# Kernel tuning notes

Hardware: AMD Instinct MI355X
Metric: run time of the kernel (lower is better)

Reference implementation:

```python
import jax, jax.numpy as jnp
import numpy as np

EPS = 1e-5

def rmsnorm(x, w):
    var = jnp.mean(x * x, axis=-1, keepdims=True)
    return x * jax.lax.rsqrt(var + EPS) * w

def apply_rope(x, cos, sin):
    # x: [B, S, H, D], cos/sin: [S, D//2]; llama-style complex rotation over pairs
    B, S, H, D = x.shape
    xr = x.reshape(B, S, H, D // 2, 2)
    x0, x1 = xr[..., 0], xr[..., 1]
    c = cos[None, :, None, :]
    s = sin[None, :, None, :]
    o0 = x0 * c - x1 * s
    o1 = x0 * s + x1 * c
    return jnp.stack([o0, o1], axis=-1).reshape(B, S, H, D)

def setup_inputs() -> dict:
    key = jax.random.key(0)
    ks = jax.random.split(key, 8)
    B, S, dim = 2, 2048, 2048
    H, nope, rope = 16, 128, 64
    q_lr, kv_lr = 1536, 512
    hd = nope + rope
    x = jax.random.normal(ks[0], (B, S, dim), jnp.float32)
    wd_q = jax.random.normal(ks[1], (dim, q_lr), jnp.float32) * (dim ** -0.5)
    wu_q = jax.random.normal(ks[2], (q_lr, H * hd), jnp.float32) * (q_lr ** -0.5)
    q_norm_w = jnp.ones((q_lr,), jnp.float32)
    wd_kv = jax.random.normal(ks[3], (dim, kv_lr + rope), jnp.float32) * (dim ** -0.5)
    wu_kv = jax.random.normal(ks[4], (kv_lr, H * 2 * nope), jnp.float32) * (kv_lr ** -0.5)
    kv_norm_w = jnp.ones((kv_lr,), jnp.float32)
    wo = jax.random.normal(ks[5], (H * nope, dim), jnp.float32) * ((H * nope) ** -0.5)
    pos = jnp.arange(S, dtype=jnp.float32)
    inv_freq = 1.0 / (10000.0 ** (jnp.arange(0, rope, 2, dtype=jnp.float32) / rope))
    ang = pos[:, None] * inv_freq[None, :]  # [S, rope//2]
    return {"x": x, "wd_q": wd_q, "wu_q": wu_q, "q_norm_w": q_norm_w,
            "wd_kv": wd_kv, "wu_kv": wu_kv, "kv_norm_w": kv_norm_w, "wo": wo,
            "cos": jnp.cos(ang), "sin": jnp.sin(ang), "start_pos": 0}

def reference(x, wd_q, wu_q, q_norm_w, wd_kv, wu_kv, kv_norm_w, wo, cos, sin, start_pos):
    B, S, dim = x.shape
    H, nope, rope = 16, 128, 64
    kv_lr = 512
    hd = nope + rope
    # low-rank Q projection + RMSNorm
    cq = x @ wd_q
    xq = rmsnorm(cq, q_norm_w) @ wu_q
    xq = xq.reshape(B, S, H, hd)
    xq_nope, xq_rope = xq[..., :nope], xq[..., nope:]
    # low-rank KV projection
    kvd = x @ wd_kv
    ckv, xk_rope = kvd[..., :kv_lr], kvd[..., kv_lr:]
    xk_rope = xk_rope.reshape(B, S, 1, rope)
    kvu = (rmsnorm(ckv, kv_norm_w) @ wu_kv).reshape(B, S, H, 2 * nope)
    xk_nope, xv = kvu[..., :nope], kvu[..., nope:]
    # partial RoPE
    xq_rope = apply_rope(xq_rope, cos, sin)
    xk_rope = apply_rope(xk_rope, cos, sin)
    xk_rope = jnp.broadcast_to(xk_rope, (B, S, H, rope))
    q = jnp.concatenate([xq_nope, xq_rope], axis=-1)  # [B,S,H,192]
    k = jnp.concatenate([xk_nope, xk_rope], axis=-1)
    # causal SDPA
    scale = 1.0 / jnp.sqrt(jnp.float32(hd))
    scores = jnp.einsum('bqhd,bkhd->bhqk', q, k) * scale
    mask = jnp.tril(jnp.ones((S, S), bool))
    scores = jnp.where(mask[None, None], scores, jnp.finfo(scores.dtype).min)
    attn = jax.nn.softmax(scores, axis=-1)
    out = jnp.einsum('bhqk,bkhd->bqhd', attn, xv).reshape(B, S, H * nope)
    return out @ wo
```

## Files before the change

kernel.cpp:

```cpp
#include <hip/hip_runtime.h>
#include <hip/hip_bf16.h>

#define S_LEN 2048
#define NHEAD 16
#define NOPE 128
#define ROPE 64
#define HD 192

typedef unsigned short ushort_t;
typedef __attribute__((ext_vector_type(8))) short short8;
typedef __attribute__((ext_vector_type(4))) float f32x4;

#define AS1 __attribute__((address_space(1)))
#define AS3 __attribute__((address_space(3)))

__device__ __forceinline__ unsigned short f2bf(float f) {
  unsigned int u = __float_as_uint(f);
  return (unsigned short)((u + 0x7FFFu + ((u >> 16) & 1u)) >> 16);
}

__global__ __launch_bounds__(256) void prep_k(const float* __restrict__ x, ushort_t* __restrict__ xb,
                                              const float* __restrict__ wd_q, ushort_t* __restrict__ wdqt,
                                              const float* __restrict__ wd_kv, ushort_t* __restrict__ wdkvt,
                                              const float* __restrict__ wu_q, ushort_t* __restrict__ wuqt,
                                              const float* __restrict__ wu_kv, ushort_t* __restrict__ wukvt,
                                              const float* __restrict__ wo, ushort_t* __restrict__ wot) {
  int id = blockIdx.x;
  if (id < 4096) {
    const int i = id * 256 + threadIdx.x;
    const float4 v0 = *(const float4*)&x[(size_t)i * 8];
    const float4 v1 = *(const float4*)&x[(size_t)i * 8 + 4];
    union { uint4 u; ushort_t s[8]; } pk;
    pk.s[0] = f2bf(v0.x); pk.s[1] = f2bf(v0.y); pk.s[2] = f2bf(v0.z); pk.s[3] = f2bf(v0.w);
    pk.s[4] = f2bf(v1.x); pk.s[5] = f2bf(v1.y); pk.s[6] = f2bf(v1.z); pk.s[7] = f2bf(v1.w);
    *(uint4*)&xb[(size_t)i * 8] = pk.u;
    return;
  }
  id -= 4096;
  const float* B; ushort_t* Bt; int K, N, gx;
  if (id < 3072)               { B = wd_q;  Bt = wdqt;  K = 2048; N = 1536; gx = 48;  }
  else if ((id -= 3072) < 1280){ B = wd_kv; Bt = wdkvt; K = 2048; N = 576;  gx = 20;  }
  else if ((id -= 1280) < 4608){ B = wu_q;  Bt = wuqt;  K = 1536; N = 3072; gx = 96;  }
  else if ((id -= 4608) < 2048){ B = wu_kv; Bt = wukvt; K = 512;  N = 4096; gx = 128; }
  else { id -= 2048;             B = wo;    Bt = wot;   K = 2048; N = 2048; gx = 64;  }
  __shared__ float tile[32][33];
  const int tx = threadIdx.x & 31, ty = threadIdx.x >> 5;
  const int n0 = (id % gx) * 32, k0 = (id / gx) * 32;
  if (n0 >= N) {
#pragma unroll
    for (int r = 0; r < 4; ++r)
      Bt[(size_t)(n0 + ty + 8 * r) * K + k0 + tx] = 0;
    return;
  }
#pragma unroll
  for (int r = 0; r < 4; ++r)
    tile[ty + 8 * r][tx] = B[(size_t)(k0 + ty + 8 * r) * N + n0 + tx];
  __syncthreads();
#pragma unroll
  for (int r = 0; r < 4; ++r)
    Bt[(size_t)(n0 + ty + 8 * r) * K + k0 + tx] = f2bf(tile[tx][ty + 8 * r]);
}

template<int EPI>
__global__ __launch_bounds__(512, 4) void mfma_gemm(const ushort_t* __restrict__ A,
                                                 const ushort_t* __restrict__ Bt,
                                                 float* __restrict__ C,
                                                 int M, int N, int K, int ldc,
                                                 ushort_t* __restrict__ kb16o,
                                                 ushort_t* __restrict__ vto,
                                                 float* __restrict__ C2,
                                                 const float* __restrict__ cosb,
                                                 const float* __restrict__ sinb) {
  __shared__ ushort_t As[128 * 32];
  __shared__ ushort_t Bs[128 * 32];
  const int tid = threadIdx.x;
  const int lane = tid & 63;
  const int wave = tid >> 6;
  const int wm = wave & 3, wn = wave >> 2;

  unsigned bxu = blockIdx.x, byu = blockIdx.y;
  {
    const unsigned gx = gridDim.x;
    const unsigned nwg = gx * gridDim.y;
    if ((nwg & 7u) == 0u) {
      unsigned flat = byu * gx + bxu;
      const unsigned cpx = nwg >> 3;
      flat = (flat & 7u) * cpx + (flat >> 3);
      bxu = flat % gx; byu = flat / gx;
    }
  }
  const int m0 = byu * 128, n0 = bxu * 128;
  const int l15 = lane & 15, quad = lane >> 4;

  f32x4 acc[2][4] = {};

  const int ma0 = tid >> 2, kc0 = tid & 3;

  typedef AS3 ushort_t lds_us;
  lds_us* AsL = (lds_us*)As;
  lds_us* BsL = (lds_us*)Bs;
  const int wbase = wave * 512;

  for (int k0 = 0; k0 < K; k0 += 32) {
    __builtin_amdgcn_global_load_lds(
        (const AS1 void*)&A[(size_t)(m0 + ma0) * K + k0 + kc0 * 8],
        (AS3 void*)(AsL + wbase), 16, 0, 0);
    __builtin_amdgcn_global_load_lds(
        (const AS1 void*)&Bt[(size_t)(n0 + ma0) * K + k0 + kc0 * 8],
        (AS3 void*)(BsL + wbase), 16, 0, 0);
    __syncthreads();

    short8 af[2], bf[4];
#pragma unroll
    for (int i = 0; i < 2; ++i)
      af[i] = *(const short8*)&As[(wm * 32 + i * 16 + l15) * 32 + quad * 8];
#pragma unroll
    for (int j = 0; j < 4; ++j)
      bf[j] = *(const short8*)&Bs[(wn * 64 + j * 16 + l15) * 32 + quad * 8];
#pragma unroll
    for (int i = 0; i < 2; ++i)
#pragma unroll
      for (int j = 0; j < 4; ++j)
        acc[i][j] = __builtin_amdgcn_mfma_f32_16x16x32_bf16(af[i], bf[j], acc[i][j], 0, 0, 0);
    __syncthreads();
  }

  if constexpr (EPI == 0) {
#pragma unroll
    for (int i = 0; i < 2; ++i)
#pragma unroll
      for (int r = 0; r < 4; ++r) {
        const size_t rg = (size_t)(m0 + wm * 32 + i * 16 + quad * 4 + r);
#pragma unroll
        for (int j = 0; j < 4; ++j)
          C[rg * ldc + n0 + wn * 64 + j * 16 + l15] = acc[i][j][r];
      }
  } else if constexpr (EPI == 1) {
    const int h = n0 >> 8;
    const bool is_v = (n0 >> 7) & 1;
    if (!is_v) {
#pragma unroll
      for (int i = 0; i < 2; ++i)
#pragma unroll
        for (int r = 0; r < 4; ++r) {
          const size_t rg = (size_t)(m0 + wm * 32 + i * 16 + quad * 4 + r);
#pragma unroll
          for (int j = 0; j < 4; ++j)
            kb16o[rg * 2048 + h * 128 + wn * 64 + j * 16 + l15] = f2bf(acc[i][j][r]);
        }
    } else {
      __shared__ __align__(16) ushort_t trb[64 * 136];
      const int bb = m0 >> 11;
      const int m0loc = m0 & 2047;
      ushort_t* vbase = vto + ((size_t)(bb * NHEAD + h) * 128) * 2048;
#pragma unroll
      for (int vh = 0; vh < 2; ++vh) {
        if (wn == vh) {
#pragma unroll
          for (int i = 0; i < 2; ++i)
#pragma unroll
            for (int r = 0; r < 4; ++r) {
              const int tloc = wm * 32 + i * 16 + quad * 4 + r;
#pragma unroll
              for (int j = 0; j < 4; ++j)
                trb[(j * 16 + l15) * 136 + tloc] = f2bf(acc[i][j][r]);
            }
        }
        __syncthreads();
#pragma unroll
        for (int it = 0; it < 2; ++it) {
          const int u = tid + (it << 9);
          const int vdl = u >> 4, tc = u & 15;
          *(uint4*)&vbase[(size_t)(vh * 64 + vdl) * 2048 + m0loc + tc * 8] =
              *(const uint4*)&trb[vdl * 136 + tc * 8];
        }
        __syncthreads();
      }
    }
  } else if constexpr (EPI == 2) {
    float* Cd;
    int ldd, nc;
    if (n0 < 1536) { Cd = C;  ldd = 1536; nc = n0; }
    else           { Cd = C2; ldd = 640;  nc = n0 - 1536; }
#pragma unroll
    for (int i = 0; i < 2; ++i)
#pragma unroll
      for (int r = 0; r < 4; ++r) {
        const size_t rg = (size_t)(m0 + wm * 32 + i * 16 + quad * 4 + r);
#pragma unroll
        for (int j = 0; j < 4; ++j)
          Cd[rg * ldd + nc + wn * 64 + j * 16 + l15] = acc[i][j][r];
      }
  } else {
    const float qscale = 0.07216878364870323f;
#pragma unroll
    for (int i = 0; i < 2; ++i)
#pragma unroll
      for (int r = 0; r < 4; ++r) {
        const int rg = m0 + wm * 32 + i * 16 + quad * 4 + r;
        const int sp = rg & (S_LEN - 1);
#pragma unroll
        for (int j = 0; j < 4; ++j) {
          const int col = n0 + wn * 64 + j * 16 + l15;
          float val = acc[i][j][r] * qscale;
          const float pr = __shfl_xor(val, 1);
          const int dd = col % HD;
          float o = val;
          if (dd >= NOPE) {
            const int d = (dd - NOPE) >> 1;
            const float cc = cosb[sp * 32 + d];
            const float sn = sinb[sp * 32 + d];
            o = (lane & 1) ? (pr * sn + val * cc) : (val * cc - pr * sn);
          }
          kb16o[(size_t)rg * 3072 + col] = f2bf(o);
        }
      }
  }
}

__global__ __launch_bounds__(256) void rmsnorm2_k(const float* __restrict__ cq,
                                                  ushort_t* __restrict__ cqn,
                                                  const float* __restrict__ qw,
                                                  const float* __restrict__ kvd,
                                                  ushort_t* __restrict__ ckvn,
                                                  const float* __restrict__ kvw,
                                                  ushort_t* __restrict__ krope16,
                                                  const float* __restrict__ cosb,
                                                  const float* __restrict__ sinb) {
  const bool is_q = blockIdx.x < 4096;
  const int row = blockIdx.x & 4095;
  const int tid = threadIdx.x;
  const float* ip = is_q ? cq + (size_t)row * 1536 : kvd + (size_t)row * 640;
  ushort_t* op = is_q ? cqn + (size_t)row * 1536 : ckvn + (size_t)row * 512;
  const float* w = is_q ? qw : kvw;
  const int L = is_q ? 1536 : 512;
  const int nper = L >> 8;
  float r[6];
  float ss = 0.f;
  for (int j = 0; j < nper; ++j) {
    r[j] = ip[tid + (j << 8)];
    ss += r[j] * r[j];
  }
  for (int off = 32; off; off >>= 1) ss += __shfl_down(ss, off);
  __shared__ float wsum[4];
  __shared__ float scale_s;
  if ((tid & 63) == 0) wsum[tid >> 6] = ss;
  __syncthreads();
  if (tid == 0) {
    float t = wsum[0] + wsum[1] + wsum[2] + wsum[3];
    scale_s = rsqrtf(t / (float)L + 1e-5f);
  }
  __syncthreads();
  const float sc = scale_s;
  for (int j = 0; j < nper; ++j)
    op[tid + (j << 8)] = f2bf(r[j] * sc * w[tid + (j << 8)]);
  if (!is_q && tid < 32) {
    const int d = tid;
    const int s = row & (S_LEN - 1);
    const float c = cosb[s * 32 + d];
    const float sn = sinb[s * 32 + d];
    const float* kb = kvd + (size_t)row * 640 + 512;
    const float y0 = kb[2 * d], y1 = kb[2 * d + 1];
    union { unsigned int u; ushort_t s2[2]; } pk;
    pk.s2[0] = f2bf(y0 * c - y1 * sn);
    pk.s2[1] = f2bf(y0 * sn + y1 * c);
    *(unsigned int*)&krope16[(size_t)row * 64 + 2 * d] = pk.u;
  }
}

#define QT 128
#define KC 64
__global__ __launch_bounds__(512, 4) void attn_k(const ushort_t* __restrict__ q16,
                                                 const ushort_t* __restrict__ kb16,
                                                 const ushort_t* __restrict__ vT,
                                                 const ushort_t* __restrict__ krope16,
                                                 ushort_t* __restrict__ outp) {
  const int bx = blockIdx.x;
  const int g = bx & 31;
  const int s = bx >> 5;
  const int tile = (s < 8) ? s : 23 - s;
  const int b = g >> 4, h = g & 15;
  const int q0 = tile * QT;
  const int tid = threadIdx.x;
  const int lane = tid & 63;
  const int wq = tid >> 6;
  const int l15 = lane & 15, quad = lane >> 4;

  __shared__ __align__(16) ushort_t Kn[64 * 128];
  __shared__ __align__(16) ushort_t Kr[64 * 64];
  __shared__ __align__(16) ushort_t Vt[2][128 * 64];
  __shared__ __align__(16) ushort_t Pb[8][16 * 72];

  const int qbase = q0 + wq * 16;
  const size_t growq = (size_t)b * S_LEN + qbase;
  const ushort_t* vTh = vT + ((size_t)(b * NHEAD + h) * 128) * 2048;
  const size_t bbase = (size_t)b * S_LEN;

  typedef AS3 ushort_t lds_us;
  lds_us* KnL = (lds_us*)Kn;
  lds_us* KrL = (lds_us*)Kr;
  lds_us* VtL = (lds_us*)Vt;
  const int wbase = wq * 512;

  auto issueK = [&](int c) {
    const size_t growk = bbase + (size_t)c * KC;
#pragma unroll
    for (int it = 0; it < 2; ++it) {
      const int u = tid + (it << 9);
      const int key = u >> 4, sl = u & 15;
      const int ss = sl ^ (key & 7);
      __builtin_amdgcn_global_load_lds(
          (const AS1 void*)&kb16[(growk + key) * 2048 + h * 128 + ss * 8],
          (AS3 void*)(KnL + wbase + it * 4096), 16, 0, 0);
    }
    {
      const int u = tid;
      const int key = u >> 3, sl = u & 7;
      const int ss = sl ^ (key & 7);
      __builtin_amdgcn_global_load_lds(
          (const AS1 void*)&krope16[(growk + key) * 64 + ss * 8],
          (AS3 void*)(KrL + wbase), 16, 0, 0);
    }
  };
  auto issueV = [&](int c, int buf) {
    const int j0 = c * KC;
#pragma unroll
    for (int it = 0; it < 2; ++it) {
      const int u = tid + (it << 9);
      const int vd = u >> 3, sl = u & 7;
      const int ss = sl ^ (vd & 7);
      __builtin_amdgcn_global_load_lds(
          (const AS1 void*)&vTh[(size_t)vd * 2048 + j0 + ss * 8],
          (AS3 void*)(VtL + buf * 8192 + wbase + it * 4096), 16, 0, 0);
    }
  };

  issueK(0);
  issueV(0, 0);
  __builtin_amdgcn_sched_barrier(0);

  short8 qf[6];
#pragma unroll
  for (int ks = 0; ks < 6; ++ks)
    qf[ks] = *(const short8*)&q16[(growq + l15) * 3072 + h * HD + ks * 32 + quad * 8];

  f32x4 oacc[8] = {};
  float mrow[4], lrow[4];
  int q_r[4];
#pragma unroll
  for (int r = 0; r < 4; ++r) {
    mrow[r] = -1e30f; lrow[r] = 0.f;
    q_r[r] = qbase + quad * 4 + r;
  }

  const int nchunk = (q0 + QT) / KC;

  asm volatile("s_waitcnt vmcnt(2)" ::: "memory");
  __builtin_amdgcn_s_barrier();
  __builtin_amdgcn_sched_barrier(0);

  for (int c = 0; c < nchunk; ++c) {
    const int j0 = c * KC;
    const bool more = (c + 1 < nchunk);
    const int buf = c & 1;
    const bool skipw = (j0 > qbase + 15);

    f32x4 sacc[4] = {};
    if (!skipw) {
      __builtin_amdgcn_s_setprio(1);
#pragma unroll
      for (int ks = 0; ks < 6; ++ks) {
        short8 kf[4];
        if (ks < 4) {
#pragma unroll
          for (int kt = 0; kt < 4; ++kt)
            kf[kt] = *(const short8*)&Kn[(kt * 16 + l15) * 128 + (((ks * 4 + quad) ^ (l15 & 7)) << 3)];
        } else {
#pragma unroll
          for (int kt = 0; kt < 4; ++kt)
            kf[kt] = *(const short8*)&Kr[(kt * 16 + l15) * 64 + ((((ks - 4) * 4 + quad) ^ (l15 & 7)) << 3)];
        }
#pragma unroll
        for (int kt = 0; kt < 4; ++kt)
          sacc[kt] = __builtin_amdgcn_mfma_f32_16x16x32_bf16(qf[ks], kf[kt], sacc[kt], 0, 0, 0);
      }
      __builtin_amdgcn_s_setprio(0);
    }

    __builtin_amdgcn_s_barrier();
    if (more) issueK(c + 1);
    __builtin_amdgcn_sched_barrier(0);

    if (!skipw) {
      if (j0 + KC - 1 > qbase) {
#pragma unroll
        for (int kt = 0; kt < 4; ++kt) {
          const int key = j0 + kt * 16 + l15;
#pragma unroll
          for (int r = 0; r < 4; ++r)
            sacc[kt][r] = (key <= q_r[r]) ? sacc[kt][r] : -1e30f;
        }
      }
      float pmax[4];
#pragma unroll
      for (int r = 0; r < 4; ++r) {
        float mx = fmaxf(fmaxf(sacc[0][r], sacc[1][r]),
                         fmaxf(sacc[2][r], sacc[3][r]));
        mx = fmaxf(mx, __shfl_xor(mx, 1));
        mx = fmaxf(mx, __shfl_xor(mx, 2));
        mx = fmaxf(mx, __shfl_xor(mx, 4));
        mx = fmaxf(mx, __shfl_xor(mx, 8));
        pmax[r] = mx;
      }
      bool need = false;
#pragma unroll
      for (int r = 0; r < 4; ++r)
        need = need || (pmax[r] > mrow[r] + 8.0f);
      const bool upd = __any(need);
      float alpha[4];
      if (upd) {
#pragma unroll
        for (int r = 0; r < 4; ++r) {
          const float mn = fmaxf(mrow[r], pmax[r]);
          alpha[r] = __expf(mrow[r] - mn);
          mrow[r] = mn;
        }
      }
#pragma unroll
      for (int kt = 0; kt < 4; ++kt)
#pragma unroll
        for (int r = 0; r < 4; ++r)
          sacc[kt][r] = __expf(sacc[kt][r] - mrow[r]);
#pragma unroll
      for (int r = 0; r < 4; ++r) {
        float rs = sacc[0][r] + sacc[1][r] + sacc[2][r] + sacc[3][r];
        rs += __shfl_xor(rs, 1);
        rs += __shfl_xor(rs, 2);
        rs += __shfl_xor(rs, 4);
        rs += __shfl_xor(rs, 8);
        lrow[r] = upd ? lrow[r] * alpha[r] + rs : lrow[r] + rs;
      }
#pragma unroll
      for (int kt = 0; kt < 4; ++kt)
#pragma unroll
        for (int r = 0; r < 4; ++r)
          Pb[wq][(quad * 4 + r) * 72 + kt * 16 + l15] = f2bf(sacc[kt][r]);
      if (upd) {
#pragma unroll
        for (int nt = 0; nt < 8; ++nt)
#pragma unroll
          for (int r = 0; r < 4; ++r)
            oacc[nt][r] *= alpha[r];
      }
    }

    if (more) asm volatile("s_waitcnt vmcnt(3)" ::: "memory");
    else      asm volatile("s_waitcnt vmcnt(0)" ::: "memory");
    __builtin_amdgcn_s_barrier();
    __builtin_amdgcn_sched_barrier(0);

    if (!skipw) {
      __builtin_amdgcn_s_setprio(1);
#pragma unroll
      for (int st = 0; st < 2; ++st) {
        const short8 pf = *(const short8*)&Pb[wq][l15 * 72 + st * 32 + quad * 8];
#pragma unroll
        for (int nt = 0; nt < 8; ++nt) {
          const short8 vf = *(const short8*)&Vt[buf][(nt * 16 + l15) * 64 + (((st * 4 + quad) ^ (l15 & 7)) << 3)];
          oacc[nt] = __builtin_amdgcn_mfma_f32_16x16x32_bf16(pf, vf, oacc[nt], 0, 0, 0);
        }
      }
      __builtin_amdgcn_s_setprio(0);
    }

    if (more) {
      issueV(c + 1, buf ^ 1);
      __builtin_amdgcn_sched_barrier(0);
      asm volatile("s_waitcnt vmcnt(2)" ::: "memory");
      __builtin_amdgcn_s_barrier();
      __builtin_amdgcn_sched_barrier(0);
    }
  }

#pragma unroll
  for (int r = 0; r < 4; ++r) {
    const float inv = 1.0f / lrow[r];
    const size_t orow = growq + quad * 4 + r;
#pragma unroll
    for (int nt = 0; nt < 8; ++nt)
      outp[orow * 2048 + h * 128 + nt * 16 + l15] = f2bf(oacc[nt][r] * inv);
  }
}

extern "C" void kernel_launch(void* const* d_in, const int* in_sizes, int n_in,
                              void* d_out, int out_size, void* d_ws, size_t ws_size,
                              hipStream_t stream) {
  const float* x        = (const float*)d_in[0];
  const float* wd_q     = (const float*)d_in[1];
  const float* wu_q     = (const float*)d_in[2];
  const float* q_norm_w = (const float*)d_in[3];
  const float* wd_kv    = (const float*)d_in[4];
  const float* wu_kv    = (const float*)d_in[5];
  const float* kv_norm_w= (const float*)d_in[6];
  const float* wo       = (const float*)d_in[7];
  const float* cosb     = (const float*)d_in[8];
  const float* sinb     = (const float*)d_in[9];
  float* out = (float*)d_out;

  char* ws = (char*)d_ws;
  float*    cq    = (float*)(ws + 0);
  ushort_t* q16   = (ushort_t*)(ws + 0);
  ushort_t* kb16  = (ushort_t*)(ws + 50331648);
  ushort_t* vT    = (ushort_t*)(ws + 67108864);
  ushort_t* xb    = (ushort_t*)(ws + 83886080);
  ushort_t* cqn   = (ushort_t*)(ws + 117440512);
  float*    kvd   = (float*)(ws + 130023424);
  ushort_t* ckvn  = (ushort_t*)(ws + 140509184);
  ushort_t* aoutb = (ushort_t*)(ws + 130023424);
  ushort_t* krope16 = (ushort_t*)(ws + 146800640);
  ushort_t* wdqt  = (ushort_t*)(ws + 147849216);
  ushort_t* wdkvt = (ushort_t*)(ws + 154140672);
  ushort_t* wuqt  = (ushort_t*)(ws + 156762112);
  ushort_t* wukvt = (ushort_t*)(ws + 166199296);
  ushort_t* wot   = (ushort_t*)(ws + 170393600);

  const int M = 2 * S_LEN;
  dim3 blk(256);
  dim3 blk512(512);

  prep_k<<<19200, blk, 0, stream>>>(x, xb, wd_q, wdqt, wd_kv, wdkvt,
                                    wu_q, wuqt, wu_kv, wukvt, wo, wot);

  mfma_gemm<2><<<dim3(2176 / 128, M / 128), blk512, 0, stream>>>(
      xb, wdqt, cq, M, 2176, 2048, 1536, nullptr, nullptr, kvd, nullptr, nullptr);
  rmsnorm2_k<<<2 * M, 256, 0, stream>>>(cq, cqn, q_norm_w, kvd, ckvn, kv_norm_w,
                                        krope16, cosb, sinb);
  mfma_gemm<3><<<dim3(3072 / 128, M / 128), blk512, 0, stream>>>(
      cqn, wuqt, nullptr, M, 3072, 1536, 0, q16, nullptr, nullptr, cosb, sinb);
  mfma_gemm<1><<<dim3(4096 / 128, M / 128), blk512, 0, stream>>>(
      ckvn, wukvt, nullptr, M, 4096, 512, 0, kb16, vT, nullptr, nullptr, nullptr);
  attn_k<<<2 * NHEAD * (S_LEN / QT), 512, 0, stream>>>(q16, kb16, vT, krope16, aoutb);
  mfma_gemm<0><<<dim3(2048 / 128, M / 128), blk512, 0, stream>>>(
      aoutb, wot, out, M, 2048, 2048, 2048, nullptr, nullptr, nullptr, nullptr, nullptr);
}
```

Baseline: 462.6 us.

## Double-buffer GEMM LDS loads with XOR swizzle and MFMA priority

Converts the bf16 MFMA GEMM main loop to a two-stage LDS double buffer, so the next K-slice's global-to-LDS loads are issued before computing on the current slice, with explicit vmcnt waits and barriers. It also XOR-swizzles the column chunk on both the load and fragment-read sides to reduce LDS bank conflicts, and raises wave priority around the MFMA block. LDS use doubles, which may lower occupancy under launch_bounds(512,4), and the hand-written waitcnt and barrier ordering has to be exactly right to stay correct.

```diff
diff --git a/kernel.cpp b/kernel.cpp
--- a/kernel.cpp
+++ b/kernel.cpp
@@ -71,8 +71,8 @@
                                                  float* __restrict__ C2,
                                                  const float* __restrict__ cosb,
                                                  const float* __restrict__ sinb) {
-  __shared__ ushort_t As[128 * 32];
-  __shared__ ushort_t Bs[128 * 32];
+  __shared__ ushort_t As[2][128 * 32];
+  __shared__ ushort_t Bs[2][128 * 32];
   const int tid = threadIdx.x;
   const int lane = tid & 63;
   const int wave = tid >> 6;
@@ -94,35 +94,57 @@
 
   f32x4 acc[2][4] = {};
 
-  const int ma0 = tid >> 2, kc0 = tid & 3;
+  const int ma0 = tid >> 2;
+  const int scol = (((tid & 3) ^ ((tid >> 3) & 3)) << 3);
+  const int rsw = (l15 >> 1) & 3;
 
   typedef AS3 ushort_t lds_us;
   lds_us* AsL = (lds_us*)As;
   lds_us* BsL = (lds_us*)Bs;
   const int wbase = wave * 512;
 
-  for (int k0 = 0; k0 < K; k0 += 32) {
+  auto issue = [&](int k0, int buf) {
     __builtin_amdgcn_global_load_lds(
-        (const AS1 void*)&A[(size_t)(m0 + ma0) * K + k0 + kc0 * 8],
-        (AS3 void*)(AsL + wbase), 16, 0, 0);
+        (const AS1 void*)&A[(size_t)(m0 + ma0) * K + k0 + scol],
+        (AS3 void*)(AsL + buf * 4096 + wbase), 16, 0, 0);
     __builtin_amdgcn_global_load_lds(
-        (const AS1 void*)&Bt[(size_t)(n0 + ma0) * K + k0 + kc0 * 8],
-        (AS3 void*)(BsL + wbase), 16, 0, 0);
-    __syncthreads();
+        (const AS1 void*)&Bt[(size_t)(n0 + ma0) * K + k0 + scol],
+        (AS3 void*)(BsL + buf * 4096 + wbase), 16, 0, 0);
+  };
+
+  const int nk = K >> 5;
+  issue(0, 0);
+  __builtin_amdgcn_sched_barrier(0);
+
+  for (int ks = 0; ks < nk; ++ks) {
+    const int buf = ks & 1;
+    const bool more = (ks + 1 < nk);
+    if (more) {
+      issue((ks + 1) << 5, buf ^ 1);
+      __builtin_amdgcn_sched_barrier(0);
+      asm volatile("s_waitcnt vmcnt(2)" ::: "memory");
+    } else {
+      asm volatile("s_waitcnt vmcnt(0)" ::: "memory");
+    }
+    __builtin_amdgcn_s_barrier();
+    __builtin_amdgcn_sched_barrier(0);
 
     short8 af[2], bf[4];
 #pragma unroll
     for (int i = 0; i < 2; ++i)
-      af[i] = *(const short8*)&As[(wm * 32 + i * 16 + l15) * 32 + quad * 8];
+      af[i] = *(const short8*)&As[buf][(wm * 32 + i * 16 + l15) * 32 + ((quad ^ rsw) << 3)];
 #pragma unroll
     for (int j = 0; j < 4; ++j)
-      bf[j] = *(const short8*)&Bs[(wn * 64 + j * 16 + l15) * 32 + quad * 8];
+      bf[j] = *(const short8*)&Bs[buf][(wn * 64 + j * 16 + l15) * 32 + ((quad ^ rsw) << 3)];
+    __builtin_amdgcn_s_setprio(1);
 #pragma unroll
     for (int i = 0; i < 2; ++i)
 #pragma unroll
       for (int j = 0; j < 4; ++j)
         acc[i][j] = __builtin_amdgcn_mfma_f32_16x16x32_bf16(af[i], bf[j], acc[i][j], 0, 0, 0);
-    __syncthreads();
+    __builtin_amdgcn_s_setprio(0);
+    __builtin_amdgcn_s_barrier();
+    __builtin_amdgcn_sched_barrier(0);
   }
 
   if constexpr (EPI == 0) {
```

Result: faster. 444.1 us (-4.0%).
